# Optimization experiments

Hardware: AMD Instinct MI355X
Metric: run time of the kernel (lower is better)

Reference implementation:

```python
import jax, jax.numpy as jnp
import numpy as np

EMBED_DIM = 768
NUM_HEADS = 12
HEAD_DIM = EMBED_DIM // NUM_HEADS
BSZ = 2
SEQ = 2048


def setup_inputs() -> dict:
    key = jax.random.key(0)
    ks = jax.random.split(key, 8)
    w = lambda k: (jax.random.normal(k, (EMBED_DIM, EMBED_DIM), jnp.float32) * 0.02)
    return {
        "hidden_states": jax.random.normal(ks[0], (BSZ, SEQ, EMBED_DIM), jnp.float32),
        "attention_mask": jnp.zeros((BSZ, 1, SEQ, SEQ), jnp.float32),
        "attention_bias": jax.random.normal(ks[1], (BSZ * NUM_HEADS, SEQ), jnp.float32),
        "Wq": w(ks[2]), "bq": jnp.zeros((EMBED_DIM,), jnp.float32),
        "Wk": w(ks[3]), "bk": jnp.zeros((EMBED_DIM,), jnp.float32),
        "Wv": w(ks[4]), "bv": jnp.zeros((EMBED_DIM,), jnp.float32),
        "Wo": w(ks[5]), "bo": jnp.zeros((EMBED_DIM,), jnp.float32),
        "beta": jnp.ones((1,), jnp.float32),
        "beta_bias": jnp.zeros((1,), jnp.float32),
    }


def reference(hidden_states, attention_mask, attention_bias, Wq, bq, Wk, bk, Wv, bv, Wo, bo, beta, beta_bias):
    b, t, e = hidden_states.shape
    scaling = HEAD_DIM ** -0.5
    split = lambda x: x.reshape(b, t, NUM_HEADS, HEAD_DIM).transpose(0, 2, 1, 3)  # b h t d
    q = split(hidden_states @ Wq.T + bq) * scaling
    k = split(hidden_states @ Wk.T + bk)
    v = split(hidden_states @ Wv.T + bv)
    # scores: [b, h, t, s]
    scores = jnp.einsum('bhqd,bhkd->bhqk', q, k)
    bias = attention_bias.reshape(b, NUM_HEADS, 1, t)  # (bsz*nh, src) -> broadcast over queries
    scores = scores + beta * bias + beta_bias + attention_mask
    probs = jax.nn.softmax(scores, axis=-1)
    out = jnp.einsum('bhqk,bhkd->bhqd', probs, v)  # b h t d
    out = out.transpose(0, 2, 1, 3).reshape(b, t, e)
    return out @ Wo.T + bo
```

## Files before the change

kernel.cpp:

```cpp
#include <hip/hip_runtime.h>
#include <hip/hip_bf16.h>

#define E 768
#define HD 64
#define NH 12
#define BSZ 2
#define SEQ 2048
#define M_ROWS (BSZ * SEQ)
#define BH (BSZ * NH)

#define LOG2E 1.44269504f
#define QSCALE 0.18033688f
#define MSHIFT 16.0f

typedef float f4_t __attribute__((ext_vector_type(4)));
typedef __bf16 bf8_t __attribute__((ext_vector_type(8)));
typedef unsigned short us8_t __attribute__((ext_vector_type(8)));
typedef unsigned short us4_t __attribute__((ext_vector_type(4)));

__device__ inline unsigned short f2bf(float f) {
  union { float f; unsigned u; } v; v.f = f;
  unsigned u = v.u + 0x7FFFu + ((v.u >> 16) & 1u);
  return (unsigned short)(u >> 16);
}

__device__ inline float ex2(float x) { return __builtin_amdgcn_exp2f(x); }

__device__ inline float bflo(unsigned u) { union { unsigned u; float f; } v; v.u = u << 16; return v.f; }
__device__ inline float bfhi(unsigned u) { union { unsigned u; float f; } v; v.u = u & 0xFFFF0000u; return v.f; }

__device__ inline unsigned pk2(float a, float b) {
  union { float f; unsigned u; } ua, ub;
  ua.f = a; ub.f = b;
  return __builtin_amdgcn_perm(ub.u + 0x8000u, ua.u + 0x8000u, 0x07060302u);
}

__global__ __launch_bounds__(256) void cvt_all(
    const float* __restrict__ X, const float* __restrict__ Wq,
    const float* __restrict__ Wk, const float* __restrict__ Wv,
    const float* __restrict__ Wo, const float* __restrict__ mask,
    unsigned short* __restrict__ Xbf, unsigned short* __restrict__ Wqkv,
    unsigned short* __restrict__ Wobf, unsigned short* __restrict__ maskbf) {
  const int nW = E * E;
  int id = blockIdx.x;
  const float* src;
  unsigned short* dst;
  float scale = 1.0f;
  int base;
  if (id < 1536) {
    src = X; dst = Xbf; base = id * 2048;
  } else if (id < 2688) {
    int r = id - 1536;
    int k = r / 288;
    int rb = r - k * 288;
    base = rb * 2048;
    if (k == 0)      { src = Wq; dst = Wqkv;          scale = QSCALE; }
    else if (k == 1) { src = Wk; dst = Wqkv + nW;     }
    else if (k == 2) { src = Wv; dst = Wqkv + 2 * nW; }
    else             { src = Wo; dst = Wobf;          }
  } else {
    src = mask; dst = maskbf; base = (id - 2688) * 2048;
  }
  int i = base + threadIdx.x * 8;
  const float4* s = (const float4*)(src + i);
  float4 a = s[0], b = s[1];
  us8_t o;
  o[0] = f2bf(a.x * scale); o[1] = f2bf(a.y * scale);
  o[2] = f2bf(a.z * scale); o[3] = f2bf(a.w * scale);
  o[4] = f2bf(b.x * scale); o[5] = f2bf(b.y * scale);
  o[6] = f2bf(b.z * scale); o[7] = f2bf(b.w * scale);
  *(us8_t*)(dst + i) = o;
}

__global__ __launch_bounds__(256) void gemm_qkv(
    const unsigned short* __restrict__ A, const unsigned short* __restrict__ Bw,
    const float* __restrict__ bq, const float* __restrict__ bk, const float* __restrict__ bv,
    unsigned short* __restrict__ Qb, unsigned short* __restrict__ Kb,
    unsigned short* __restrict__ Vtb) {
  __shared__ unsigned short Alds[64 * 64];
  __shared__ unsigned short Blds[128 * 64];
  const int w = threadIdx.x >> 6, lane = threadIdx.x & 63;
  const int quad = lane >> 4, l15 = lane & 15;
  const int rowBase = blockIdx.x * 64;
  const int colBase = blockIdx.y * 128;
  const int wr = (w & 1) * 32, wc = (w >> 1) * 64;
  f4_t acc[2][4] = {};
  const int swz = l15 & 7;

  for (int k0 = 0; k0 < E; k0 += 64) {
    __syncthreads();
#pragma unroll
    for (int c = 0; c < 2; ++c) {
      int s = c * 256 + w * 64 + lane;
      int r = s >> 3, col = ((s & 7) ^ (r & 7)) * 8;
      const unsigned short* ga = A + (size_t)(rowBase + r) * E + k0 + col;
      __builtin_amdgcn_global_load_lds((const __attribute__((address_space(1))) void*)ga,
          (__attribute__((address_space(3))) void*)&Alds[c * 2048 + w * 512], 16, 0, 0);
    }
#pragma unroll
    for (int c = 0; c < 4; ++c) {
      int s = c * 256 + w * 64 + lane;
      int r = s >> 3, col = ((s & 7) ^ (r & 7)) * 8;
      const unsigned short* gb = Bw + (size_t)(colBase + r) * E + k0 + col;
      __builtin_amdgcn_global_load_lds((const __attribute__((address_space(1))) void*)gb,
          (__attribute__((address_space(3))) void*)&Blds[c * 2048 + w * 512], 16, 0, 0);
    }
    __builtin_amdgcn_s_waitcnt(0);
    __syncthreads();
    bf8_t af[2][2], bfr[4][2];
#pragma unroll
    for (int mi = 0; mi < 2; ++mi)
#pragma unroll
      for (int ks = 0; ks < 2; ++ks)
        af[mi][ks] = *(const bf8_t*)&Alds[(wr + mi * 16 + l15) * 64 + (((ks * 4 + quad) ^ swz) << 3)];
#pragma unroll
    for (int ni = 0; ni < 4; ++ni)
#pragma unroll
      for (int ks = 0; ks < 2; ++ks)
        bfr[ni][ks] = *(const bf8_t*)&Blds[(wc + ni * 16 + l15) * 64 + (((ks * 4 + quad) ^ swz) << 3)];
#pragma unroll
    for (int ks = 0; ks < 2; ++ks)
#pragma unroll
      for (int mi = 0; mi < 2; ++mi)
#pragma unroll
        for (int ni = 0; ni < 4; ++ni)
          acc[mi][ni] = __builtin_amdgcn_mfma_f32_16x16x32_bf16(af[mi][ks], bfr[ni][ks], acc[mi][ni], 0, 0, 0);
  }

  const int which = colBase / E;
  __syncthreads();
  if (which < 2) {
    const float* biasP = (which == 0) ? bq : bk;
    unsigned short* dst = (which == 0) ? Qb : Kb;
    const float bscale = (which == 0) ? QSCALE : 1.0f;
    const int cnBase = colBase - which * E + wc;
    const int h = cnBase >> 6;
    float biasv[4];
#pragma unroll
    for (int ni = 0; ni < 4; ++ni) biasv[ni] = biasP[cnBase + ni * 16 + l15] * bscale;
    unsigned short* T = Blds + w * 1024;
    const int row = lane >> 2, colE = (lane & 3) * 16;
#pragma unroll
    for (int mi = 0; mi < 2; ++mi) {
#pragma unroll
      for (int ni = 0; ni < 4; ++ni)
#pragma unroll
        for (int r = 0; r < 4; ++r)
          T[(quad * 4 + r) * 64 + ni * 16 + l15] = f2bf(acc[mi][ni][r] + biasv[ni]);
      us8_t o0 = *(const us8_t*)&T[row * 64 + colE];
      us8_t o1 = *(const us8_t*)&T[row * 64 + colE + 8];
      int gm = rowBase + wr + mi * 16 + row;
      int b = gm >> 11, t = gm & 2047;
      unsigned short* drow = dst + ((size_t)(b * NH + h) * SEQ + t) * HD;
      *(us8_t*)&drow[colE] = o0;
      *(us8_t*)&drow[colE + 8] = o1;
    }
  } else {
#pragma unroll
    for (int mi = 0; mi < 2; ++mi) {
#pragma unroll
      for (int ni = 0; ni < 4; ++ni) {
        int cn = colBase - 2 * E + wc + ni * 16 + l15;
        int h = cn >> 6, d = cn & 63;
        float bias = bv[cn];
        int gm0 = rowBase + wr + mi * 16 + quad * 4;
        int b = gm0 >> 11, t = gm0 & 2047;
        us4_t o4;
#pragma unroll
        for (int r = 0; r < 4; ++r) o4[r] = f2bf(acc[mi][ni][r] + bias);
        *(us4_t*)&Vtb[((size_t)(b * NH + h) * HD + d) * SEQ + t] = o4;
      }
    }
  }
}

__global__ __launch_bounds__(256, 4) void flash_attn11(
    const unsigned short* __restrict__ Qb, const unsigned short* __restrict__ Kb,
    const unsigned short* __restrict__ Vt, const float* __restrict__ biasArr,
    const unsigned short* __restrict__ maskB, const float* __restrict__ betaP,
    unsigned short* __restrict__ attn) {
  __shared__ __align__(16) char smem[24576];
  unsigned short* Klds = (unsigned short*)smem;
  unsigned short* Vlds = (unsigned short*)(smem + 8192);
  unsigned short* Plds = (unsigned short*)(smem + 16384);
  const int tid = threadIdx.x;
  const int w = tid >> 6, lane = tid & 63;
  const int quad = lane >> 4, l15 = lane & 15;
  const int id = blockIdx.x;
  const int h = id >> 6;
  const int qb = id & 63;
  const int qt = qb >> 1, b = qb & 1;
  const int bh = b * NH + h;
  const int q0 = qt * 64;
  const int q = q0 + w * 16 + l15;
  const float betav2 = betaP[0] * LOG2E;
  const int sw = l15 & 7;

  const unsigned short* qbase = Qb + ((size_t)bh * SEQ + q) * HD;
  bf8_t qf[2];
  qf[0] = *(const bf8_t*)(qbase + quad * 8);
  qf[1] = *(const bf8_t*)(qbase + 32 + quad * 8);

  union { us8_t u; bf8_t b; } ou;
#pragma unroll
  for (int i = 0; i < 8; ++i) ou.u[i] = 0x3F80;
  const bf8_t ones = ou.b;

  f4_t Oacc[4] = {};
  f4_t Lacc = {};

  unsigned short* Pw = Plds + w * 1024;
  const unsigned short* KgBase = Kb + (size_t)bh * SEQ * HD;
  const unsigned short* VtG = Vt + (size_t)bh * HD * SEQ;
  const unsigned short* maskRow = maskB + ((size_t)b * SEQ + q) * SEQ;
  const float* biasRow = biasArr + (size_t)bh * SEQ;

  const int e0 = tid * 8;
  const int r0 = e0 >> 6, c0 = e0 & 63;
  const int e1 = 2048 + e0;
  const int r1 = e1 >> 6, c1 = e1 & 63;
  const int ph0 = r0 * 64 + ((((c0 >> 3) ^ (r0 & 7))) << 3);
  const int ph1 = r1 * 64 + ((((c1 >> 3) ^ (r1 & 7))) << 3);

  us8_t kreg0, kreg1, vreg0, vreg1;
  uint2 mregu[4];

  {
    const unsigned short* pk0 = KgBase + (size_t)r0 * HD + c0;
    const unsigned short* pk1 = KgBase + (size_t)r1 * HD + c1;
    const unsigned short* pv0 = VtG + (size_t)r0 * SEQ + c0;
    const unsigned short* pv1 = VtG + (size_t)r1 * SEQ + c1;
    asm volatile(
        "global_load_dwordx4 %0, %4, off\n\t"
        "global_load_dwordx4 %1, %5, off\n\t"
        "global_load_dwordx4 %2, %6, off\n\t"
        "global_load_dwordx4 %3, %7, off"
        : "=&v"(kreg0), "=&v"(kreg1), "=&v"(vreg0), "=&v"(vreg1)
        : "v"(pk0), "v"(pk1), "v"(pv0), "v"(pv1));
  }
#pragma unroll
  for (int st = 0; st < 4; ++st)
    mregu[st] = *(const uint2*)&maskRow[st * 16 + quad * 4];

  for (int it = 0; it < 32; ++it) {
    const int soff = it * 64;
    asm volatile("s_waitcnt vmcnt(0)"
                 : "+v"(kreg0), "+v"(kreg1), "+v"(vreg0), "+v"(vreg1));
    __syncthreads();
    *(us8_t*)&Klds[ph0] = kreg0;
    *(us8_t*)&Klds[ph1] = kreg1;
    *(us8_t*)&Vlds[ph0] = vreg0;
    *(us8_t*)&Vlds[ph1] = vreg1;
    __syncthreads();

    float4 bb[4];
#pragma unroll
    for (int st = 0; st < 4; ++st) {
      float4 b4 = *(const float4*)&biasRow[soff + st * 16 + quad * 4];
      bb[st].x = fmaf(betav2, b4.x, -MSHIFT);
      bb[st].y = fmaf(betav2, b4.y, -MSHIFT);
      bb[st].z = fmaf(betav2, b4.z, -MSHIFT);
      bb[st].w = fmaf(betav2, b4.w, -MSHIFT);
    }

    f4_t sacc[4];
#pragma unroll
    for (int st = 0; st < 4; ++st) {
      sacc[st] = (f4_t){0.f, 0.f, 0.f, 0.f};
#pragma unroll
      for (int ks = 0; ks < 2; ++ks) {
        bf8_t kf = *(const bf8_t*)&Klds[(st * 16 + l15) * 64 + (((ks * 4 + quad) ^ sw) << 3)];
        sacc[st] = __builtin_amdgcn_mfma_f32_16x16x32_bf16(kf, qf[ks], sacc[st], 0, 0, 0);
      }
    }

#pragma unroll
    for (int st = 0; st < 4; ++st) {
      sacc[st][0] += fmaf(LOG2E, bflo(mregu[st].x), bb[st].x);
      sacc[st][1] += fmaf(LOG2E, bfhi(mregu[st].x), bb[st].y);
      sacc[st][2] += fmaf(LOG2E, bflo(mregu[st].y), bb[st].z);
      sacc[st][3] += fmaf(LOG2E, bfhi(mregu[st].y), bb[st].w);
    }

    if (it < 31) {
      const int nf = soff + 64;
      const unsigned short* pk0 = KgBase + (size_t)(nf + r0) * HD + c0;
      const unsigned short* pk1 = KgBase + (size_t)(nf + r1) * HD + c1;
      const unsigned short* pv0 = VtG + (size_t)r0 * SEQ + nf + c0;
      const unsigned short* pv1 = VtG + (size_t)r1 * SEQ + nf + c1;
      asm volatile(
          "global_load_dwordx4 %0, %4, off\n\t"
          "global_load_dwordx4 %1, %5, off\n\t"
          "global_load_dwordx4 %2, %6, off\n\t"
          "global_load_dwordx4 %3, %7, off"
          : "=&v"(kreg0), "=&v"(kreg1), "=&v"(vreg0), "=&v"(vreg1)
          : "v"(pk0), "v"(pk1), "v"(pv0), "v"(pv1));
#pragma unroll
      for (int st = 0; st < 4; ++st)
        mregu[st] = *(const uint2*)&maskRow[nf + st * 16 + quad * 4];
    }

#pragma unroll
    for (int st = 0; st < 4; ++st)
#pragma unroll
      for (int r = 0; r < 4; ++r) sacc[st][r] = ex2(sacc[st][r]);

#pragma unroll
    for (int st = 0; st < 4; ++st) {
      uint2 pp;
      pp.x = pk2(sacc[st][0], sacc[st][1]);
      pp.y = pk2(sacc[st][2], sacc[st][3]);
      int col = st * 16 + quad * 4;
      int addr = l15 * 64 + ((((col >> 3) ^ sw)) << 3) + (col & 7);
      *(uint2*)&Pw[addr] = pp;
    }

#pragma unroll
    for (int ks = 0; ks < 2; ++ks) {
      bf8_t pf = *(const bf8_t*)&Pw[l15 * 64 + (((ks * 4 + quad) ^ sw) << 3)];
      Lacc = __builtin_amdgcn_mfma_f32_16x16x32_bf16(ones, pf, Lacc, 0, 0, 0);
#pragma unroll
      for (int dt = 0; dt < 4; ++dt) {
        bf8_t vf = *(const bf8_t*)&Vlds[(dt * 16 + l15) * 64 + (((ks * 4 + quad) ^ sw) << 3)];
        Oacc[dt] = __builtin_amdgcn_mfma_f32_16x16x32_bf16(vf, pf, Oacc[dt], 0, 0, 0);
      }
    }
  }

  float inv = 1.0f / Lacc[0];
  unsigned short* orow = attn + ((size_t)b * SEQ + q) * E + h * HD;
#pragma unroll
  for (int dt = 0; dt < 4; ++dt) {
    us4_t o4;
#pragma unroll
    for (int r = 0; r < 4; ++r) o4[r] = f2bf(Oacc[dt][r] * inv);
    *(us4_t*)&orow[dt * 16 + quad * 4] = o4;
  }
}

__global__ __launch_bounds__(256) void gemm_out(
    const unsigned short* __restrict__ A, const unsigned short* __restrict__ Bw,
    const float* __restrict__ bo, float* __restrict__ out) {
  __shared__ unsigned short Alds[64 * 64];
  __shared__ unsigned short Blds[64 * 64];
  const int w = threadIdx.x >> 6, lane = threadIdx.x & 63;
  const int quad = lane >> 4, l15 = lane & 15;
  const int rowBase = blockIdx.x * 64;
  const int colBase = blockIdx.y * 64;
  const int wr = (w & 1) * 32, wc = (w >> 1) * 32;
  f4_t acc[2][2] = {};
  const int swz = l15 & 7;

  for (int k0 = 0; k0 < E; k0 += 64) {
    __syncthreads();
#pragma unroll
    for (int c = 0; c < 2; ++c) {
      int s = c * 256 + w * 64 + lane;
      int r = s >> 3, col = ((s & 7) ^ (r & 7)) * 8;
      const unsigned short* ga = A + (size_t)(rowBase + r) * E + k0 + col;
      __builtin_amdgcn_global_load_lds((const __attribute__((address_space(1))) void*)ga,
          (__attribute__((address_space(3))) void*)&Alds[c * 2048 + w * 512], 16, 0, 0);
      const unsigned short* gb = Bw + (size_t)(colBase + r) * E + k0 + col;
      __builtin_amdgcn_global_load_lds((const __attribute__((address_space(1))) void*)gb,
          (__attribute__((address_space(3))) void*)&Blds[c * 2048 + w * 512], 16, 0, 0);
    }
    __builtin_amdgcn_s_waitcnt(0);
    __syncthreads();
    bf8_t af[2][2], bfr[2][2];
#pragma unroll
    for (int mi = 0; mi < 2; ++mi)
#pragma unroll
      for (int ks = 0; ks < 2; ++ks)
        af[mi][ks] = *(const bf8_t*)&Alds[(wr + mi * 16 + l15) * 64 + (((ks * 4 + quad) ^ swz) << 3)];
#pragma unroll
    for (int ni = 0; ni < 2; ++ni)
#pragma unroll
      for (int ks = 0; ks < 2; ++ks)
        bfr[ni][ks] = *(const bf8_t*)&Blds[(wc + ni * 16 + l15) * 64 + (((ks * 4 + quad) ^ swz) << 3)];
#pragma unroll
    for (int ks = 0; ks < 2; ++ks)
#pragma unroll
      for (int mi = 0; mi < 2; ++mi)
#pragma unroll
        for (int ni = 0; ni < 2; ++ni)
          acc[mi][ni] = __builtin_amdgcn_mfma_f32_16x16x32_bf16(af[mi][ks], bfr[ni][ks], acc[mi][ni], 0, 0, 0);
  }

#pragma unroll
  for (int mi = 0; mi < 2; ++mi) {
#pragma unroll
    for (int ni = 0; ni < 2; ++ni) {
      int gn = colBase + wc + ni * 16 + l15;
      float bias = bo[gn];
#pragma unroll
      for (int r = 0; r < 4; ++r) {
        int gm = rowBase + wr + mi * 16 + quad * 4 + r;
        out[(size_t)gm * E + gn] = acc[mi][ni][r] + bias;
      }
    }
  }
}

extern "C" void kernel_launch(void* const* d_in, const int* in_sizes, int n_in,
                              void* d_out, int out_size, void* d_ws, size_t ws_size,
                              hipStream_t stream) {
  const float* hidden = (const float*)d_in[0];
  const float* mask = (const float*)d_in[1];
  const float* abias = (const float*)d_in[2];
  const float* Wq = (const float*)d_in[3];
  const float* bq = (const float*)d_in[4];
  const float* Wk = (const float*)d_in[5];
  const float* bk = (const float*)d_in[6];
  const float* Wv = (const float*)d_in[7];
  const float* bv = (const float*)d_in[8];
  const float* Wo = (const float*)d_in[9];
  const float* bo = (const float*)d_in[10];
  const float* beta = (const float*)d_in[11];
  float* out = (float*)d_out;

  char* ws = (char*)d_ws;
  unsigned short* Xbf = (unsigned short*)(ws);
  unsigned short* Wqkv = (unsigned short*)(ws + 6291456);
  unsigned short* Wobf = (unsigned short*)(ws + 9830400);
  unsigned short* Qbuf = (unsigned short*)(ws + 11010048);
  unsigned short* Kbuf = (unsigned short*)(ws + 17301504);
  unsigned short* Vtb = (unsigned short*)(ws + 23592960);
  unsigned short* Maskbf = (unsigned short*)(ws + 29884416);
  unsigned short* Attn = Xbf;

  cvt_all<<<6784, 256, 0, stream>>>(hidden, Wq, Wk, Wv, Wo, mask, Xbf, Wqkv, Wobf, Maskbf);
  gemm_qkv<<<dim3(64, 18), 256, 0, stream>>>(Xbf, Wqkv, bq, bk, bv, Qbuf, Kbuf, Vtb);
  flash_attn11<<<768, 256, 0, stream>>>(Qbuf, Kbuf, Vtb, abias, Maskbf, beta, Attn);
  gemm_out<<<dim3(64, 12), 256, 0, stream>>>(Attn, Wobf, bo, out);
}
```

Baseline: 226.7 us.

## Overlap mask conversion with QKV GEMM and issue mask loads via inline asm

Mask fp32-to-bf16 conversion moves out of the initial conversion kernel and into extra blocks appended to the QKV GEMM launch. Those blocks can run alongside the GEMM tiles instead of in a separate serial step, which flattens the GEMM grid to 1D. In the attention kernel, the mask prefetch loads go into the same inline-asm batch as the K/V loads and share one vmcnt wait, so the compiler cannot insert early waits on them. The risk is that memory-bound mask blocks compete with the GEMM for bandwidth and CUs.

```diff
diff --git a/kernel.cpp b/kernel.cpp
--- a/kernel.cpp
+++ b/kernel.cpp
@@ -35,12 +35,11 @@
   return __builtin_amdgcn_perm(ub.u + 0x8000u, ua.u + 0x8000u, 0x07060302u);
 }
 
-__global__ __launch_bounds__(256) void cvt_all(
+__global__ __launch_bounds__(256) void cvt_xw(
     const float* __restrict__ X, const float* __restrict__ Wq,
     const float* __restrict__ Wk, const float* __restrict__ Wv,
-    const float* __restrict__ Wo, const float* __restrict__ mask,
-    unsigned short* __restrict__ Xbf, unsigned short* __restrict__ Wqkv,
-    unsigned short* __restrict__ Wobf, unsigned short* __restrict__ maskbf) {
+    const float* __restrict__ Wo, unsigned short* __restrict__ Xbf,
+    unsigned short* __restrict__ Wqkv, unsigned short* __restrict__ Wobf) {
   const int nW = E * E;
   int id = blockIdx.x;
   const float* src;
@@ -49,7 +48,7 @@
   int base;
   if (id < 1536) {
     src = X; dst = Xbf; base = id * 2048;
-  } else if (id < 2688) {
+  } else {
     int r = id - 1536;
     int k = r / 288;
     int rb = r - k * 288;
@@ -58,8 +57,6 @@
     else if (k == 1) { src = Wk; dst = Wqkv + nW;     }
     else if (k == 2) { src = Wv; dst = Wqkv + 2 * nW; }
     else             { src = Wo; dst = Wobf;          }
-  } else {
-    src = mask; dst = maskbf; base = (id - 2688) * 2048;
   }
   int i = base + threadIdx.x * 8;
   const float4* s = (const float4*)(src + i);
@@ -72,17 +69,30 @@
   *(us8_t*)(dst + i) = o;
 }
 
-__global__ __launch_bounds__(256) void gemm_qkv(
+__global__ __launch_bounds__(256) void gemm_qkv_maskcvt(
     const unsigned short* __restrict__ A, const unsigned short* __restrict__ Bw,
     const float* __restrict__ bq, const float* __restrict__ bk, const float* __restrict__ bv,
     unsigned short* __restrict__ Qb, unsigned short* __restrict__ Kb,
-    unsigned short* __restrict__ Vtb) {
+    unsigned short* __restrict__ Vtb, const float* __restrict__ mask,
+    unsigned short* __restrict__ maskbf) {
   __shared__ unsigned short Alds[64 * 64];
   __shared__ unsigned short Blds[128 * 64];
+
+  if (blockIdx.x >= 1152) {
+    int base = (blockIdx.x - 1152) * 2048 + threadIdx.x * 8;
+    const float4* s = (const float4*)(mask + base);
+    float4 a = s[0], b = s[1];
+    us8_t o;
+    o[0] = f2bf(a.x); o[1] = f2bf(a.y); o[2] = f2bf(a.z); o[3] = f2bf(a.w);
+    o[4] = f2bf(b.x); o[5] = f2bf(b.y); o[6] = f2bf(b.z); o[7] = f2bf(b.w);
+    *(us8_t*)(maskbf + base) = o;
+    return;
+  }
+
   const int w = threadIdx.x >> 6, lane = threadIdx.x & 63;
   const int quad = lane >> 4, l15 = lane & 15;
-  const int rowBase = blockIdx.x * 64;
-  const int colBase = blockIdx.y * 128;
+  const int rowBase = (blockIdx.x & 63) * 64;
+  const int colBase = (blockIdx.x >> 6) * 128;
   const int wr = (w & 1) * 32, wc = (w >> 1) * 64;
   f4_t acc[2][4] = {};
   const int swz = l15 & 7;
@@ -174,7 +184,7 @@
   }
 }
 
-__global__ __launch_bounds__(256, 4) void flash_attn11(
+__global__ __launch_bounds__(256, 4) void flash_attn12(
     const unsigned short* __restrict__ Qb, const unsigned short* __restrict__ Kb,
     const unsigned short* __restrict__ Vt, const float* __restrict__ biasArr,
     const unsigned short* __restrict__ maskB, const float* __restrict__ betaP,
@@ -223,29 +233,37 @@
   const int ph1 = r1 * 64 + ((((c1 >> 3) ^ (r1 & 7))) << 3);
 
   us8_t kreg0, kreg1, vreg0, vreg1;
-  uint2 mregu[4];
+  uint2 m0, m1, m2, m3;
 
   {
     const unsigned short* pk0 = KgBase + (size_t)r0 * HD + c0;
     const unsigned short* pk1 = KgBase + (size_t)r1 * HD + c1;
     const unsigned short* pv0 = VtG + (size_t)r0 * SEQ + c0;
     const unsigned short* pv1 = VtG + (size_t)r1 * SEQ + c1;
+    const unsigned short* pm0 = maskRow + quad * 4;
+    const unsigned short* pm1 = maskRow + 16 + quad * 4;
+    const unsigned short* pm2 = maskRow + 32 + quad * 4;
+    const unsigned short* pm3 = maskRow + 48 + quad * 4;
     asm volatile(
-        "global_load_dwordx4 %0, %4, off\n\t"
-        "global_load_dwordx4 %1, %5, off\n\t"
-        "global_load_dwordx4 %2, %6, off\n\t"
-        "global_load_dwordx4 %3, %7, off"
-        : "=&v"(kreg0), "=&v"(kreg1), "=&v"(vreg0), "=&v"(vreg1)
-        : "v"(pk0), "v"(pk1), "v"(pv0), "v"(pv1));
-  }
-#pragma unroll
-  for (int st = 0; st < 4; ++st)
-    mregu[st] = *(const uint2*)&maskRow[st * 16 + quad * 4];
+        "global_load_dwordx4 %0, %8, off\n\t"
+        "global_load_dwordx4 %1, %9, off\n\t"
+        "global_load_dwordx4 %2, %10, off\n\t"
+        "global_load_dwordx4 %3, %11, off\n\t"
+        "global_load_dwordx2 %4, %12, off\n\t"
+        "global_load_dwordx2 %5, %13, off\n\t"
+        "global_load_dwordx2 %6, %14, off\n\t"
+        "global_load_dwordx2 %7, %15, off"
+        : "=&v"(kreg0), "=&v"(kreg1), "=&v"(vreg0), "=&v"(vreg1),
+          "=&v"(m0), "=&v"(m1), "=&v"(m2), "=&v"(m3)
+        : "v"(pk0), "v"(pk1), "v"(pv0), "v"(pv1),
+          "v"(pm0), "v"(pm1), "v"(pm2), "v"(pm3));
+  }
 
   for (int it = 0; it < 32; ++it) {
     const int soff = it * 64;
     asm volatile("s_waitcnt vmcnt(0)"
-                 : "+v"(kreg0), "+v"(kreg1), "+v"(vreg0), "+v"(vreg1));
+                 : "+v"(kreg0), "+v"(kreg1), "+v"(vreg0), "+v"(vreg1),
+                   "+v"(m0), "+v"(m1), "+v"(m2), "+v"(m3));
     __syncthreads();
     *(us8_t*)&Klds[ph0] = kreg0;
     *(us8_t*)&Klds[ph1] = kreg1;
@@ -274,13 +292,22 @@
       }
     }
 
-#pragma unroll
-    for (int st = 0; st < 4; ++st) {
-      sacc[st][0] += fmaf(LOG2E, bflo(mregu[st].x), bb[st].x);
-      sacc[st][1] += fmaf(LOG2E, bfhi(mregu[st].x), bb[st].y);
-      sacc[st][2] += fmaf(LOG2E, bflo(mregu[st].y), bb[st].z);
-      sacc[st][3] += fmaf(LOG2E, bfhi(mregu[st].y), bb[st].w);
-    }
+    sacc[0][0] += fmaf(LOG2E, bflo(m0.x), bb[0].x);
+    sacc[0][1] += fmaf(LOG2E, bfhi(m0.x), bb[0].y);
+    sacc[0][2] += fmaf(LOG2E, bflo(m0.y), bb[0].z);
+    sacc[0][3] += fmaf(LOG2E, bfhi(m0.y), bb[0].w);
+    sacc[1][0] += fmaf(LOG2E, bflo(m1.x), bb[1].x);
+    sacc[1][1] += fmaf(LOG2E, bfhi(m1.x), bb[1].y);
+    sacc[1][2] += fmaf(LOG2E, bflo(m1.y), bb[1].z);
+    sacc[1][3] += fmaf(LOG2E, bfhi(m1.y), bb[1].w);
+    sacc[2][0] += fmaf(LOG2E, bflo(m2.x), bb[2].x);
+    sacc[2][1] += fmaf(LOG2E, bfhi(m2.x), bb[2].y);
+    sacc[2][2] += fmaf(LOG2E, bflo(m2.y), bb[2].z);
+    sacc[2][3] += fmaf(LOG2E, bfhi(m2.y), bb[2].w);
+    sacc[3][0] += fmaf(LOG2E, bflo(m3.x), bb[3].x);
+    sacc[3][1] += fmaf(LOG2E, bfhi(m3.x), bb[3].y);
+    sacc[3][2] += fmaf(LOG2E, bflo(m3.y), bb[3].z);
+    sacc[3][3] += fmaf(LOG2E, bfhi(m3.y), bb[3].w);
 
     if (it < 31) {
       const int nf = soff + 64;
@@ -288,16 +315,23 @@
       const unsigned short* pk1 = KgBase + (size_t)(nf + r1) * HD + c1;
       const unsigned short* pv0 = VtG + (size_t)r0 * SEQ + nf + c0;
       const unsigned short* pv1 = VtG + (size_t)r1 * SEQ + nf + c1;
+      const unsigned short* pm0 = maskRow + nf + quad * 4;
+      const unsigned short* pm1 = maskRow + nf + 16 + quad * 4;
+      const unsigned short* pm2 = maskRow + nf + 32 + quad * 4;
+      const unsigned short* pm3 = maskRow + nf + 48 + quad * 4;
       asm volatile(
-          "global_load_dwordx4 %0, %4, off\n\t"
-          "global_load_dwordx4 %1, %5, off\n\t"
-          "global_load_dwordx4 %2, %6, off\n\t"
-          "global_load_dwordx4 %3, %7, off"
-          : "=&v"(kreg0), "=&v"(kreg1), "=&v"(vreg0), "=&v"(vreg1)
-          : "v"(pk0), "v"(pk1), "v"(pv0), "v"(pv1));
-#pragma unroll
-      for (int st = 0; st < 4; ++st)
-        mregu[st] = *(const uint2*)&maskRow[nf + st * 16 + quad * 4];
+          "global_load_dwordx4 %0, %8, off\n\t"
+          "global_load_dwordx4 %1, %9, off\n\t"
+          "global_load_dwordx4 %2, %10, off\n\t"
+          "global_load_dwordx4 %3, %11, off\n\t"
+          "global_load_dwordx2 %4, %12, off\n\t"
+          "global_load_dwordx2 %5, %13, off\n\t"
+          "global_load_dwordx2 %6, %14, off\n\t"
+          "global_load_dwordx2 %7, %15, off"
+          : "=&v"(kreg0), "=&v"(kreg1), "=&v"(vreg0), "=&v"(vreg1),
+            "=&v"(m0), "=&v"(m1), "=&v"(m2), "=&v"(m3)
+          : "v"(pk0), "v"(pk1), "v"(pv0), "v"(pv1),
+            "v"(pm0), "v"(pm1), "v"(pm2), "v"(pm3));
     }
 
 #pragma unroll
@@ -428,8 +462,8 @@
   unsigned short* Maskbf = (unsigned short*)(ws + 29884416);
   unsigned short* Attn = Xbf;
 
-  cvt_all<<<6784, 256, 0, stream>>>(hidden, Wq, Wk, Wv, Wo, mask, Xbf, Wqkv, Wobf, Maskbf);
-  gemm_qkv<<<dim3(64, 18), 256, 0, stream>>>(Xbf, Wqkv, bq, bk, bv, Qbuf, Kbuf, Vtb);
-  flash_attn11<<<768, 256, 0, stream>>>(Qbuf, Kbuf, Vtb, abias, Maskbf, beta, Attn);
+  cvt_xw<<<2688, 256, 0, stream>>>(hidden, Wq, Wk, Wv, Wo, Xbf, Wqkv, Wobf);
+  gemm_qkv_maskcvt<<<5248, 256, 0, stream>>>(Xbf, Wqkv, bq, bk, bv, Qbuf, Kbuf, Vtb, mask, Maskbf);
+  flash_attn12<<<768, 256, 0, stream>>>(Qbuf, Kbuf, Vtb, abias, Maskbf, beta, Attn);
   gemm_out<<<dim3(64, 12), 256, 0, stream>>>(Attn, Wobf, bo, out);
 }
```

Measured after the change: 235.6 us. 3.9% more time.

## Double-buffer K/V tiles in LDS with one barrier per iteration

Applied to the files above, without the earlier changes.

The attention kernel now keeps two LDS buffers for K and V. The next tile is written into the alternate buffer during the current iteration, and the global prefetch runs two tiles ahead. This drops one of the two __syncthreads per iteration and the wait on global loads at the top of each loop. In exchange LDS use rises from 24KB to 40KB per block, which may reduce how many blocks fit on a CU, and the store to LDS still waits on vmcnt(0) in the middle of the iteration.

```diff
diff --git a/kernel.cpp b/kernel.cpp
--- a/kernel.cpp
+++ b/kernel.cpp
@@ -174,15 +174,15 @@
   }
 }
 
-__global__ __launch_bounds__(256, 4) void flash_attn11(
+__global__ __launch_bounds__(256, 4) void flash_attn13(
     const unsigned short* __restrict__ Qb, const unsigned short* __restrict__ Kb,
     const unsigned short* __restrict__ Vt, const float* __restrict__ biasArr,
     const unsigned short* __restrict__ maskB, const float* __restrict__ betaP,
     unsigned short* __restrict__ attn) {
-  __shared__ __align__(16) char smem[24576];
-  unsigned short* Klds = (unsigned short*)smem;
-  unsigned short* Vlds = (unsigned short*)(smem + 8192);
-  unsigned short* Plds = (unsigned short*)(smem + 16384);
+  __shared__ __align__(16) char smem[40960];
+  unsigned short* Kbase = (unsigned short*)smem;
+  unsigned short* Vbase = (unsigned short*)(smem + 16384);
+  unsigned short* Plds = (unsigned short*)(smem + 32768);
   const int tid = threadIdx.x;
   const int w = tid >> 6, lane = tid & 63;
   const int quad = lane >> 4, l15 = lane & 15;
@@ -241,17 +241,31 @@
 #pragma unroll
   for (int st = 0; st < 4; ++st)
     mregu[st] = *(const uint2*)&maskRow[st * 16 + quad * 4];
+  asm volatile("s_waitcnt vmcnt(0)"
+               : "+v"(kreg0), "+v"(kreg1), "+v"(vreg0), "+v"(vreg1));
+  *(us8_t*)&Kbase[ph0] = kreg0;
+  *(us8_t*)&Kbase[ph1] = kreg1;
+  *(us8_t*)&Vbase[ph0] = vreg0;
+  *(us8_t*)&Vbase[ph1] = vreg1;
+  __syncthreads();
+  {
+    const unsigned short* pk0 = KgBase + (size_t)(64 + r0) * HD + c0;
+    const unsigned short* pk1 = KgBase + (size_t)(64 + r1) * HD + c1;
+    const unsigned short* pv0 = VtG + (size_t)r0 * SEQ + 64 + c0;
+    const unsigned short* pv1 = VtG + (size_t)r1 * SEQ + 64 + c1;
+    asm volatile(
+        "global_load_dwordx4 %0, %4, off\n\t"
+        "global_load_dwordx4 %1, %5, off\n\t"
+        "global_load_dwordx4 %2, %6, off\n\t"
+        "global_load_dwordx4 %3, %7, off"
+        : "=&v"(kreg0), "=&v"(kreg1), "=&v"(vreg0), "=&v"(vreg1)
+        : "v"(pk0), "v"(pk1), "v"(pv0), "v"(pv1));
+  }
 
   for (int it = 0; it < 32; ++it) {
     const int soff = it * 64;
-    asm volatile("s_waitcnt vmcnt(0)"
-                 : "+v"(kreg0), "+v"(kreg1), "+v"(vreg0), "+v"(vreg1));
-    __syncthreads();
-    *(us8_t*)&Klds[ph0] = kreg0;
-    *(us8_t*)&Klds[ph1] = kreg1;
-    *(us8_t*)&Vlds[ph0] = vreg0;
-    *(us8_t*)&Vlds[ph1] = vreg1;
-    __syncthreads();
+    unsigned short* Kc = Kbase + (it & 1) * 4096;
+    unsigned short* Vc = Vbase + (it & 1) * 4096;
 
     float4 bb[4];
 #pragma unroll
@@ -269,7 +283,7 @@
       sacc[st] = (f4_t){0.f, 0.f, 0.f, 0.f};
 #pragma unroll
       for (int ks = 0; ks < 2; ++ks) {
-        bf8_t kf = *(const bf8_t*)&Klds[(st * 16 + l15) * 64 + (((ks * 4 + quad) ^ sw) << 3)];
+        bf8_t kf = *(const bf8_t*)&Kc[(st * 16 + l15) * 64 + (((ks * 4 + quad) ^ sw) << 3)];
         sacc[st] = __builtin_amdgcn_mfma_f32_16x16x32_bf16(kf, qf[ks], sacc[st], 0, 0, 0);
       }
     }
@@ -282,28 +296,38 @@
       sacc[st][3] += fmaf(LOG2E, bfhi(mregu[st].y), bb[st].w);
     }
 
+#pragma unroll
+    for (int st = 0; st < 4; ++st)
+#pragma unroll
+      for (int r = 0; r < 4; ++r) sacc[st][r] = ex2(sacc[st][r]);
+
     if (it < 31) {
-      const int nf = soff + 64;
-      const unsigned short* pk0 = KgBase + (size_t)(nf + r0) * HD + c0;
-      const unsigned short* pk1 = KgBase + (size_t)(nf + r1) * HD + c1;
-      const unsigned short* pv0 = VtG + (size_t)r0 * SEQ + nf + c0;
-      const unsigned short* pv1 = VtG + (size_t)r1 * SEQ + nf + c1;
-      asm volatile(
-          "global_load_dwordx4 %0, %4, off\n\t"
-          "global_load_dwordx4 %1, %5, off\n\t"
-          "global_load_dwordx4 %2, %6, off\n\t"
-          "global_load_dwordx4 %3, %7, off"
-          : "=&v"(kreg0), "=&v"(kreg1), "=&v"(vreg0), "=&v"(vreg1)
-          : "v"(pk0), "v"(pk1), "v"(pv0), "v"(pv1));
+      asm volatile("s_waitcnt vmcnt(0)"
+                   : "+v"(kreg0), "+v"(kreg1), "+v"(vreg0), "+v"(vreg1));
+      unsigned short* Kn = Kbase + ((it + 1) & 1) * 4096;
+      unsigned short* Vn = Vbase + ((it + 1) & 1) * 4096;
+      *(us8_t*)&Kn[ph0] = kreg0;
+      *(us8_t*)&Kn[ph1] = kreg1;
+      *(us8_t*)&Vn[ph0] = vreg0;
+      *(us8_t*)&Vn[ph1] = vreg1;
+      if (it < 30) {
+        const int nf = soff + 128;
+        const unsigned short* pk0 = KgBase + (size_t)(nf + r0) * HD + c0;
+        const unsigned short* pk1 = KgBase + (size_t)(nf + r1) * HD + c1;
+        const unsigned short* pv0 = VtG + (size_t)r0 * SEQ + nf + c0;
+        const unsigned short* pv1 = VtG + (size_t)r1 * SEQ + nf + c1;
+        asm volatile(
+            "global_load_dwordx4 %0, %4, off\n\t"
+            "global_load_dwordx4 %1, %5, off\n\t"
+            "global_load_dwordx4 %2, %6, off\n\t"
+            "global_load_dwordx4 %3, %7, off"
+            : "=&v"(kreg0), "=&v"(kreg1), "=&v"(vreg0), "=&v"(vreg1)
+            : "v"(pk0), "v"(pk1), "v"(pv0), "v"(pv1));
+      }
 #pragma unroll
       for (int st = 0; st < 4; ++st)
-        mregu[st] = *(const uint2*)&maskRow[nf + st * 16 + quad * 4];
-    }
-
-#pragma unroll
-    for (int st = 0; st < 4; ++st)
-#pragma unroll
-      for (int r = 0; r < 4; ++r) sacc[st][r] = ex2(sacc[st][r]);
+        mregu[st] = *(const uint2*)&maskRow[soff + 64 + st * 16 + quad * 4];
+    }
 
 #pragma unroll
     for (int st = 0; st < 4; ++st) {
@@ -321,10 +345,12 @@
       Lacc = __builtin_amdgcn_mfma_f32_16x16x32_bf16(ones, pf, Lacc, 0, 0, 0);
 #pragma unroll
       for (int dt = 0; dt < 4; ++dt) {
-        bf8_t vf = *(const bf8_t*)&Vlds[(dt * 16 + l15) * 64 + (((ks * 4 + quad) ^ sw) << 3)];
+        bf8_t vf = *(const bf8_t*)&Vc[(dt * 16 + l15) * 64 + (((ks * 4 + quad) ^ sw) << 3)];
         Oacc[dt] = __builtin_amdgcn_mfma_f32_16x16x32_bf16(vf, pf, Oacc[dt], 0, 0, 0);
       }
     }
+
+    __syncthreads();
   }
 
   float inv = 1.0f / Lacc[0];
@@ -430,6 +456,6 @@
 
   cvt_all<<<6784, 256, 0, stream>>>(hidden, Wq, Wk, Wv, Wo, mask, Xbf, Wqkv, Wobf, Maskbf);
   gemm_qkv<<<dim3(64, 18), 256, 0, stream>>>(Xbf, Wqkv, bq, bk, bv, Qbuf, Kbuf, Vtb);
-  flash_attn11<<<768, 256, 0, stream>>>(Qbuf, Kbuf, Vtb, abias, Maskbf, beta, Attn);
+  flash_attn13<<<768, 256, 0, stream>>>(Qbuf, Kbuf, Vtb, abias, Maskbf, beta, Attn);
   gemm_out<<<dim3(64, 12), 256, 0, stream>>>(Attn, Wobf, bo, out);
 }
```

Measured after the change: 244.6 us. 1.08x slower.
